# Optimization experiments

Measured on AMD Instinct MI355X. Metric: run time of the kernel, lower is better.

The kernel has to match this reference:

```python
import jax, jax.numpy as jnp
import numpy as np

B, S = 4096, 2048
MTU = 1500.0
# per-profile targets (hard-coded dicts in the original forward)
TARGET_DELAY = jnp.array([2.0, 1.0, 0.5, 5.0, 3.0], dtype=jnp.float32)
TARGET_PAD = jnp.array([0.08, 0.12, 0.05, 0.15, 0.10], dtype=jnp.float32)
# deterministic stand-in for random.choice over 4 DpiConfigs: per-config sensitivity
CONFIG_MULT = jnp.array([1.0, 1.3, 1.6, 2.0], dtype=jnp.float32)

DPI_W, SIM_W, EFF_W, CONF_W = 2.0, 0.5, 0.3, 0.2
MAX_DELAY_MS, MAX_PAD = 20.0, 0.3


def _dpi_scores(sizes_f, delays_f, dirs_f, padding_norm, delay_ms, profile_ids):
    # Original detaches padding/delay before the (non-differentiable) DPI sim.
    pad = jax.lax.stop_gradient(padding_norm)
    dly = jax.lax.stop_gradient(delay_ms)
    sizes_f = jax.lax.stop_gradient(sizes_f)
    delays_f = jax.lax.stop_gradient(delays_f)
    # last-packet morphing: add padding bytes (capped at MTU) and applied delay
    sizes_f = sizes_f.at[:, -1].set(jnp.minimum(sizes_f[:, -1] + pad * MTU, MTU))
    delays_f = delays_f.at[:, -1].add(dly)
    # stateful per-packet suspicion heuristics, expressed via shifted prev-packet views
    prev_size = jnp.concatenate([jnp.full((sizes_f.shape[0], 1), -1.0, sizes_f.dtype), sizes_f[:, :-1]], axis=1)
    prev_dir = jnp.concatenate([jnp.full((dirs_f.shape[0], 1), -1.0, dirs_f.dtype), dirs_f[:, :-1]], axis=1)
    inc = (0.6 * (sizes_f > 1400.0)
           + 0.4 * (delays_f < 0.05)
           + 0.2 * (jnp.abs(sizes_f - prev_size) < 0.5)
           + 0.1 * (dirs_f != prev_dir)).astype(jnp.float32)
    base = inc.mean(axis=1) * 100.0  # [B] suspicion score in ~[0, 100]
    mult = CONFIG_MULT[(profile_ids % 4).astype(jnp.int32)]
    return base * mult


def setup_inputs() -> dict:
    key = jax.random.key(0)
    ks = jax.random.split(key, 7)
    return {
        'raw_sizes': jax.random.randint(ks[0], (B, S), 0, 1500, dtype=jnp.int32),
        'raw_delays': jax.random.uniform(ks[1], (B, S), dtype=jnp.float32) * 10.0,
        'raw_directions': jax.random.randint(ks[2], (B, S), 0, 2, dtype=jnp.int32),
        'delay_ms': jax.random.uniform(ks[3], (B,), dtype=jnp.float32) * 30.0,
        'padding_norm': jax.random.uniform(ks[4], (B,), dtype=jnp.float32),
        'confidence': jax.random.uniform(ks[5], (B,), dtype=jnp.float32),
        'profile_ids': jax.random.randint(ks[6], (B,), 0, 5, dtype=jnp.int64),
    }


def reference(raw_sizes, raw_delays, raw_directions, delay_ms, padding_norm, confidence, profile_ids):
    scores = _dpi_scores(raw_sizes.astype(jnp.float32), raw_delays,
                         raw_directions.astype(jnp.float32),
                         padding_norm, delay_ms, profile_ids)
    dpi_loss = jax.nn.relu(scores - 15.0).mean() / 30.0
    pid = profile_ids.astype(jnp.int32)
    similarity_loss = (jnp.abs(delay_ms - TARGET_DELAY[pid]) + jnp.abs(padding_norm - TARGET_PAD[pid])).mean()
    efficiency_loss = jax.nn.relu(delay_ms - MAX_DELAY_MS).mean() / MAX_DELAY_MS + jax.nn.relu(padding_norm - MAX_PAD).mean()
    evasion_rate = (scores < 30.0).astype(jnp.float32)
    confidence_loss = jnp.mean((confidence - evasion_rate) ** 2)
    total = DPI_W * dpi_loss + SIM_W * similarity_loss + EFF_W * efficiency_loss + CONF_W * confidence_loss
    return total
```

## Files before the change

kernel.cpp:

```cpp
#include <hip/hip_runtime.h>

#define BLOCK 256

__device__ __constant__ float c_target_delay[5] = {2.0f, 1.0f, 0.5f, 5.0f, 3.0f};
__device__ __constant__ float c_target_pad[5]   = {0.08f, 0.12f, 0.05f, 0.15f, 0.10f};
__device__ __constant__ float c_config_mult[4]  = {1.0f, 1.3f, 1.6f, 2.0f};

__global__ __launch_bounds__(BLOCK) void row_loss_kernel(
    const int*   __restrict__ sizes,
    const float* __restrict__ delays,
    const int*   __restrict__ dirs,
    const float* __restrict__ delay_ms,
    const float* __restrict__ pad_norm,
    const float* __restrict__ conf,
    const int*   __restrict__ pids,
    float*       __restrict__ row_out,
    int S, float invB)
{
    const int r    = blockIdx.x;
    const int tid  = threadIdx.x;
    const int lane = tid & 63;
    const int wv   = tid >> 6;
    const int base = tid * 8;
    const long long rowoff = (long long)r * (long long)S;

    const int*   srow = sizes  + rowoff;
    const float* drow = delays + rowoff;
    const int*   grow = dirs   + rowoff;

    const float pad = pad_norm[r];
    const float dly = delay_ms[r];

    const int4*   sv = (const int4*)(srow + base);
    const float4* dv = (const float4*)(drow + base);
    const int4*   gv = (const int4*)(grow + base);
    int4   s0 = sv[0], s1 = sv[1];
    float4 d0 = dv[0], d1 = dv[1];
    int4   g0 = gv[0], g1 = gv[1];

    float sz[8] = {(float)s0.x, (float)s0.y, (float)s0.z, (float)s0.w,
                   (float)s1.x, (float)s1.y, (float)s1.z, (float)s1.w};
    float dl[8] = {d0.x, d0.y, d0.z, d0.w, d1.x, d1.y, d1.z, d1.w};
    float dr[8] = {(float)g0.x, (float)g0.y, (float)g0.z, (float)g0.w,
                   (float)g1.x, (float)g1.y, (float)g1.z, (float)g1.w};

    const float rawsz7 = sz[7], rawdr7 = dr[7];
    float psz = __shfl_up(rawsz7, 1, 64);
    float pdr = __shfl_up(rawdr7, 1, 64);

    __shared__ float wl_sz[BLOCK / 64], wl_dr[BLOCK / 64];
    if (lane == 63) { wl_sz[wv] = rawsz7; wl_dr[wv] = rawdr7; }
    __syncthreads();
    if (lane == 0) {
        if (tid == 0) { psz = -1.0f; pdr = -1.0f; }
        else          { psz = wl_sz[wv - 1]; pdr = wl_dr[wv - 1]; }
    }

    if (base + 8 == S) {
        sz[7] = fminf(sz[7] + pad * 1500.0f, 1500.0f);
        dl[7] = dl[7] + dly;
    }

    float sum = 0.0f;
    #pragma unroll
    for (int j = 0; j < 8; ++j) {
        float inc = 0.0f;
        inc += (sz[j] > 1400.0f)           ? 0.6f : 0.0f;
        inc += (dl[j] < 0.05f)             ? 0.4f : 0.0f;
        inc += (fabsf(sz[j] - psz) < 0.5f) ? 0.2f : 0.0f;
        inc += (dr[j] != pdr)              ? 0.1f : 0.0f;
        sum += inc;
        psz = sz[j];
        pdr = dr[j];
    }

    #pragma unroll
    for (int off = 32; off > 0; off >>= 1)
        sum += __shfl_down(sum, off, 64);

    __shared__ float wsum[BLOCK / 64];
    if (lane == 0) wsum[wv] = sum;
    __syncthreads();

    if (tid == 0) {
        float tot = 0.0f;
        #pragma unroll
        for (int w = 0; w < BLOCK / 64; ++w) tot += wsum[w];

        const int pid = pids[r];
        const float mult  = c_config_mult[pid & 3];
        const float score = tot * (100.0f / (float)S) * mult;

        float v = 0.0f;
        v += (2.0f / 30.0f) * fmaxf(score - 15.0f, 0.0f);
        v += 0.5f * (fabsf(dly - c_target_delay[pid]) +
                     fabsf(pad - c_target_pad[pid]));
        v += (0.3f / 20.0f) * fmaxf(dly - 20.0f, 0.0f);
        v += 0.3f * fmaxf(pad - 0.3f, 0.0f);
        const float ev = (score < 30.0f) ? 1.0f : 0.0f;
        const float c  = conf[r] - ev;
        v += 0.2f * c * c;

        row_out[r] = v * invB;
    }
}

__global__ __launch_bounds__(BLOCK) void reduce_kernel(
    const float* __restrict__ row, float* __restrict__ out, int B)
{
    const int tid = threadIdx.x;
    float s = 0.0f;
    for (int i = tid; i < B; i += BLOCK) s += row[i];

    #pragma unroll
    for (int off = 32; off > 0; off >>= 1)
        s += __shfl_down(s, off, 64);

    __shared__ float wsum[BLOCK / 64];
    if ((tid & 63) == 0) wsum[tid >> 6] = s;
    __syncthreads();

    if (tid == 0) {
        float tot = 0.0f;
        #pragma unroll
        for (int w = 0; w < BLOCK / 64; ++w) tot += wsum[w];
        out[0] = tot;
    }
}

extern "C" void kernel_launch(void* const* d_in, const int* in_sizes, int n_in,
                              void* d_out, int out_size, void* d_ws, size_t ws_size,
                              hipStream_t stream) {
    const int*   sizes    = (const int*)  d_in[0];
    const float* delays   = (const float*)d_in[1];
    const int*   dirs     = (const int*)  d_in[2];
    const float* delay_ms = (const float*)d_in[3];
    const float* pad_norm = (const float*)d_in[4];
    const float* conf     = (const float*)d_in[5];
    const int*   pids     = (const int*)  d_in[6];
    float* out = (float*)d_out;

    const int B = in_sizes[3];
    const int S = in_sizes[0] / B;

    float* row_ws = (float*)d_ws;

    row_loss_kernel<<<B, BLOCK, 0, stream>>>(
        sizes, delays, dirs, delay_ms, pad_norm, conf, pids,
        row_ws, S, 1.0f / (float)B);

    reduce_kernel<<<1, BLOCK, 0, stream>>>(row_ws, out, B);
}
```

Baseline: 26.20 us.

## Remove block barriers: per-wave partial sums, move per-row loss into final kernel

The row kernel no longer uses shared memory or __syncthreads. Each wave loads its own previous-boundary element straight from global memory and writes its per-segment partial sum to workspace. All per-row loss math (score, similarity, efficiency, confidence) moves into a single 1024-thread final kernel that reads the four partials as a float4. This cuts barrier stalls in the bandwidth-bound main kernel, but adds a larger serial final kernel on one block and hard-codes the segment layout to S=2048 with 4 segments.

```diff
diff --git a/kernel.cpp b/kernel.cpp
--- a/kernel.cpp
+++ b/kernel.cpp
@@ -6,37 +6,32 @@
 __device__ __constant__ float c_target_pad[5]   = {0.08f, 0.12f, 0.05f, 0.15f, 0.10f};
 __device__ __constant__ float c_config_mult[4]  = {1.0f, 1.3f, 1.6f, 2.0f};
 
-__global__ __launch_bounds__(BLOCK) void row_loss_kernel(
+__global__ __launch_bounds__(BLOCK) void seg_kernel(
     const int*   __restrict__ sizes,
     const float* __restrict__ delays,
     const int*   __restrict__ dirs,
     const float* __restrict__ delay_ms,
     const float* __restrict__ pad_norm,
-    const float* __restrict__ conf,
-    const int*   __restrict__ pids,
-    float*       __restrict__ row_out,
-    int S, float invB)
+    float*       __restrict__ partial,
+    int S)
 {
-    const int r    = blockIdx.x;
-    const int tid  = threadIdx.x;
-    const int lane = tid & 63;
-    const int wv   = tid >> 6;
-    const int base = tid * 8;
-    const long long rowoff = (long long)r * (long long)S;
+    const int lane = threadIdx.x & 63;
+    const int seg  = threadIdx.x >> 6;
+    const int row  = blockIdx.x;
+    const long long rowoff = (long long)row * (long long)S;
+    const int segbase = seg * 512;
+    const int base = segbase + lane * 8;
 
     const int*   srow = sizes  + rowoff;
     const float* drow = delays + rowoff;
     const int*   grow = dirs   + rowoff;
 
-    const float pad = pad_norm[r];
-    const float dly = delay_ms[r];
-
-    const int4*   sv = (const int4*)(srow + base);
-    const float4* dv = (const float4*)(drow + base);
-    const int4*   gv = (const int4*)(grow + base);
-    int4   s0 = sv[0], s1 = sv[1];
-    float4 d0 = dv[0], d1 = dv[1];
-    int4   g0 = gv[0], g1 = gv[1];
+    int4   s0 = ((const int4*)(srow + base))[0];
+    int4   s1 = ((const int4*)(srow + base))[1];
+    float4 d0 = ((const float4*)(drow + base))[0];
+    float4 d1 = ((const float4*)(drow + base))[1];
+    int4   g0 = ((const int4*)(grow + base))[0];
+    int4   g1 = ((const int4*)(grow + base))[1];
 
     float sz[8] = {(float)s0.x, (float)s0.y, (float)s0.z, (float)s0.w,
                    (float)s1.x, (float)s1.y, (float)s1.z, (float)s1.w};
@@ -44,21 +39,19 @@
     float dr[8] = {(float)g0.x, (float)g0.y, (float)g0.z, (float)g0.w,
                    (float)g1.x, (float)g1.y, (float)g1.z, (float)g1.w};
 
-    const float rawsz7 = sz[7], rawdr7 = dr[7];
-    float psz = __shfl_up(rawsz7, 1, 64);
-    float pdr = __shfl_up(rawdr7, 1, 64);
-
-    __shared__ float wl_sz[BLOCK / 64], wl_dr[BLOCK / 64];
-    if (lane == 63) { wl_sz[wv] = rawsz7; wl_dr[wv] = rawdr7; }
-    __syncthreads();
+    float psz = __shfl_up(sz[7], 1, 64);
+    float pdr = __shfl_up(dr[7], 1, 64);
     if (lane == 0) {
-        if (tid == 0) { psz = -1.0f; pdr = -1.0f; }
-        else          { psz = wl_sz[wv - 1]; pdr = wl_dr[wv - 1]; }
+        if (seg == 0) { psz = -1.0f; pdr = -1.0f; }
+        else {
+            psz = (float)srow[segbase - 1];
+            pdr = (float)grow[segbase - 1];
+        }
     }
 
-    if (base + 8 == S) {
-        sz[7] = fminf(sz[7] + pad * 1500.0f, 1500.0f);
-        dl[7] = dl[7] + dly;
+    if (seg == 3 && lane == 63) {
+        sz[7] = fminf(sz[7] + pad_norm[row] * 1500.0f, 1500.0f);
+        dl[7] = dl[7] + delay_ms[row];
     }
 
     float sum = 0.0f;
@@ -78,18 +71,29 @@
     for (int off = 32; off > 0; off >>= 1)
         sum += __shfl_down(sum, off, 64);
 
-    __shared__ float wsum[BLOCK / 64];
-    if (lane == 0) wsum[wv] = sum;
-    __syncthreads();
+    if (lane == 0) partial[row * 4 + seg] = sum;
+}
 
-    if (tid == 0) {
-        float tot = 0.0f;
-        #pragma unroll
-        for (int w = 0; w < BLOCK / 64; ++w) tot += wsum[w];
+__global__ __launch_bounds__(1024) void final_kernel(
+    const float* __restrict__ partial,
+    const float* __restrict__ delay_ms,
+    const float* __restrict__ pad_norm,
+    const float* __restrict__ conf,
+    const int*   __restrict__ pids,
+    float*       __restrict__ out,
+    int B, float inv_s_x100, float invB)
+{
+    const int tid = threadIdx.x;
+    float s = 0.0f;
 
-        const int pid = pids[r];
-        const float mult  = c_config_mult[pid & 3];
-        const float score = tot * (100.0f / (float)S) * mult;
+    for (int r = tid; r < B; r += 1024) {
+        float4 p = ((const float4*)partial)[r];
+        const float tot = (p.x + p.y) + (p.z + p.w);
+
+        const int   pid = pids[r];
+        const float dly = delay_ms[r];
+        const float pad = pad_norm[r];
+        const float score = tot * inv_s_x100 * c_config_mult[pid & 3];
 
         float v = 0.0f;
         v += (2.0f / 30.0f) * fmaxf(score - 15.0f, 0.0f);
@@ -101,29 +105,21 @@
         const float c  = conf[r] - ev;
         v += 0.2f * c * c;
 
-        row_out[r] = v * invB;
+        s += v * invB;
     }
-}
-
-__global__ __launch_bounds__(BLOCK) void reduce_kernel(
-    const float* __restrict__ row, float* __restrict__ out, int B)
-{
-    const int tid = threadIdx.x;
-    float s = 0.0f;
-    for (int i = tid; i < B; i += BLOCK) s += row[i];
 
     #pragma unroll
     for (int off = 32; off > 0; off >>= 1)
         s += __shfl_down(s, off, 64);
 
-    __shared__ float wsum[BLOCK / 64];
+    __shared__ float wsum[1024 / 64];
     if ((tid & 63) == 0) wsum[tid >> 6] = s;
     __syncthreads();
 
     if (tid == 0) {
         float tot = 0.0f;
         #pragma unroll
-        for (int w = 0; w < BLOCK / 64; ++w) tot += wsum[w];
+        for (int w = 0; w < 1024 / 64; ++w) tot += wsum[w];
         out[0] = tot;
     }
 }
@@ -143,11 +139,12 @@
     const int B = in_sizes[3];
     const int S = in_sizes[0] / B;
 
-    float* row_ws = (float*)d_ws;
+    float* partial = (float*)d_ws;
 
-    row_loss_kernel<<<B, BLOCK, 0, stream>>>(
-        sizes, delays, dirs, delay_ms, pad_norm, conf, pids,
-        row_ws, S, 1.0f / (float)B);
+    seg_kernel<<<B, BLOCK, 0, stream>>>(
+        sizes, delays, dirs, delay_ms, pad_norm, partial, S);
 
-    reduce_kernel<<<1, BLOCK, 0, stream>>>(row_ws, out, B);
+    final_kernel<<<1, 1024, 0, stream>>>(
+        partial, delay_ms, pad_norm, conf, pids, out,
+        B, 100.0f / (float)S, 1.0f / (float)B);
 }
```

New measurement: 24.97 us, median of 2. -4.7%, faster.
